# Optimization experiments

Measured on AMD Instinct MI355X. Metric: run time of the kernel, lower is better.

The kernel has to match this reference:

```python
import jax, jax.numpy as jnp
import numpy as np

D_MODEL = 1024
N_HEADS = 16
HEAD_DIM = D_MODEL // N_HEADS


def setup_inputs() -> dict:
    key = jax.random.key(0)
    ks = jax.random.split(key, 9)
    B, S = 2, 2048
    s = 1.0 / np.sqrt(D_MODEL)
    return {
        "x": jax.random.normal(ks[0], (B, S, D_MODEL), dtype=jnp.float32),
        "Wq": jax.random.normal(ks[1], (D_MODEL, D_MODEL), dtype=jnp.float32) * s,
        "bq": jnp.zeros((D_MODEL,), dtype=jnp.float32),
        "Wk": jax.random.normal(ks[2], (D_MODEL, D_MODEL), dtype=jnp.float32) * s,
        "bk": jnp.zeros((D_MODEL,), dtype=jnp.float32),
        "Wv": jax.random.normal(ks[3], (D_MODEL, D_MODEL), dtype=jnp.float32) * s,
        "bv": jnp.zeros((D_MODEL,), dtype=jnp.float32),
        "Wo": jax.random.normal(ks[4], (D_MODEL, D_MODEL), dtype=jnp.float32) * s,
        "bo": jnp.zeros((D_MODEL,), dtype=jnp.float32),
    }


def _rope_emb(seq_len, dtype):
    # inv_freq over even dims of head_dim; emb = cat(freqs, freqs)
    inv_freq = 1.0 / (10000.0 ** (jnp.arange(0, HEAD_DIM, 2, dtype=jnp.float32) / HEAD_DIM))
    t = jnp.arange(seq_len, dtype=jnp.float32)
    freqs = t[:, None] * inv_freq[None, :]          # [S, head_dim/2]
    emb = jnp.concatenate([freqs, freqs], axis=-1)  # [S, head_dim]
    return emb.astype(dtype)[None, None, :, :]       # [1,1,S,head_dim]


def _rotate_half(x):
    x1, x2 = jnp.split(x, 2, axis=-1)
    return jnp.concatenate([-x2, x1], axis=-1)


def _apply_rope(x, emb):
    return x * jnp.cos(emb) + _rotate_half(x) * jnp.sin(emb)


def reference(x, Wq, bq, Wk, bk, Wv, bv, Wo, bo):
    B, S, _ = x.shape
    # projections (torch Linear: x @ W.T + b; here W is stored already as [in,out])
    q = (x @ Wq + bq).reshape(B, S, N_HEADS, HEAD_DIM).transpose(0, 2, 1, 3)
    k = (x @ Wk + bk).reshape(B, S, N_HEADS, HEAD_DIM).transpose(0, 2, 1, 3)
    v = (x @ Wv + bv).reshape(B, S, N_HEADS, HEAD_DIM).transpose(0, 2, 1, 3)
    emb = _rope_emb(S, x.dtype)
    q = _apply_rope(q, emb)
    k = _apply_rope(k, emb)
    scores = jnp.einsum('bhqd,bhkd->bhqk', q, k) / jnp.sqrt(jnp.asarray(HEAD_DIM, x.dtype))
    attn = jax.nn.softmax(scores, axis=-1)
    out = jnp.einsum('bhqk,bhkd->bhqd', attn, v)
    out = out.transpose(0, 2, 1, 3).reshape(B, S, D_MODEL)
    return out @ Wo + bo
```

## Files before the change

kernel.cpp:

```cpp
#include <hip/hip_runtime.h>
#include <hip/hip_bf16.h>
#include <math.h>

#define SEQ 2048
#define DM 1024
#define NH 16
#define HD 64
#define NBH 32
#define MTOT 4096

typedef __attribute__((ext_vector_type(8))) short short8;
typedef __attribute__((ext_vector_type(4))) float floatx4;
typedef __attribute__((ext_vector_type(8))) unsigned short u16x8;
typedef __attribute__((ext_vector_type(4))) unsigned short u16x4;

__device__ __forceinline__ unsigned short f2bf(float f) {
    unsigned int u = __float_as_uint(f);
    u += 0x7FFFu + ((u >> 16) & 1u);
    return (unsigned short)(u >> 16);
}

#define AS1C const __attribute__((address_space(1))) void*
#define AS3  __attribute__((address_space(3))) void*

#define QSCALE 0.18033688011112042f

__global__ __launch_bounds__(256) void cvt_x_kernel(
    const float* __restrict__ x, unsigned short* __restrict__ xb)
{
    size_t base = ((size_t)blockIdx.x * 256 + threadIdx.x) * 8;
    float4 a = *(const float4*)(x + base);
    float4 b = *(const float4*)(x + base + 4);
    u16x8 o;
    o[0]=f2bf(a.x); o[1]=f2bf(a.y); o[2]=f2bf(a.z); o[3]=f2bf(a.w);
    o[4]=f2bf(b.x); o[5]=f2bf(b.y); o[6]=f2bf(b.z); o[7]=f2bf(b.w);
    *(u16x8*)(xb + base) = o;
}

__global__ __launch_bounds__(256) void cvt_w_kernel(
    const float* __restrict__ Wq, const float* __restrict__ Wk,
    const float* __restrict__ Wv, const float* __restrict__ Wo,
    unsigned short* __restrict__ Wt)
{
    __shared__ float Ls[64][65];
    const int z = blockIdx.z;
    const float* src = (z==0) ? Wq : (z==1) ? Wk : (z==2) ? Wv : Wo;
    unsigned short* dst = Wt + (size_t)z * DM * DM;
    const int tid = threadIdx.x;
    const int k0 = blockIdx.x * 64, n0 = blockIdx.y * 64;

    int r = tid >> 2, cseg = (tid & 3) * 16;
    #pragma unroll
    for (int e = 0; e < 4; ++e) {
        float4 v = *(const float4*)(src + (size_t)(k0 + r) * DM + n0 + cseg + e*4);
        Ls[r][cseg+e*4+0] = v.x; Ls[r][cseg+e*4+1] = v.y;
        Ls[r][cseg+e*4+2] = v.z; Ls[r][cseg+e*4+3] = v.w;
    }
    __syncthreads();
    int n = tid >> 2, kseg = (tid & 3) * 16;
    #pragma unroll
    for (int half = 0; half < 2; ++half) {
        u16x8 o;
        #pragma unroll
        for (int e = 0; e < 8; ++e) o[e] = f2bf(Ls[kseg + half*8 + e][n]);
        *(u16x8*)(dst + (size_t)(n0 + n) * DM + k0 + kseg + half*8) = o;
    }
}

#define GEMM_CORE(A_, Bt_, m0_, n0_)                                          \
    const int tid = threadIdx.x;                                              \
    const int wave = tid >> 6, lane = tid & 63;                               \
    const int quad = lane >> 4, l16 = lane & 15;                              \
    const int mh = (wave & 1) * 64, nh = (wave >> 1) * 64;                    \
    floatx4 acc[4][4];                                                        \
    _Pragma("unroll")                                                         \
    for (int i = 0; i < 4; ++i)                                               \
        _Pragma("unroll")                                                     \
        for (int j = 0; j < 4; ++j) acc[i][j] = (floatx4){0.f,0.f,0.f,0.f};   \
    {                                                                         \
        const int srow = wave*32 + (lane>>2);                                 \
        const int scol = (lane & 3) * 8;                                      \
        const unsigned short* ga = A_ + (size_t)(m0_ + srow)*DM + scol;       \
        const unsigned short* gb = Bt_ + (size_t)(n0_ + srow)*DM + scol;      \
        char* lA = (char*)As; char* lB = (char*)Bs;                           \
        for (int k0 = 0; k0 < DM; k0 += 32) {                                 \
            __syncthreads();                                                  \
            _Pragma("unroll")                                                 \
            for (int u = 0; u < 2; ++u) {                                     \
                __builtin_amdgcn_global_load_lds(                             \
                    (AS1C)(ga + (size_t)u*16*DM + k0),                        \
                    (AS3)(lA + (wave*32 + u*16)*64), 16, 0, 0);               \
                __builtin_amdgcn_global_load_lds(                             \
                    (AS1C)(gb + (size_t)u*16*DM + k0),                        \
                    (AS3)(lB + (wave*32 + u*16)*64), 16, 0, 0);               \
            }                                                                 \
            __syncthreads();                                                  \
            short8 af[4], bf[4];                                              \
            _Pragma("unroll")                                                 \
            for (int t = 0; t < 4; ++t) {                                     \
                af[t] = *(const short8*)&As[(mh + t*16 + l16)*32 + quad*8];   \
                bf[t] = *(const short8*)&Bs[(nh + t*16 + l16)*32 + quad*8];   \
            }                                                                 \
            _Pragma("unroll")                                                 \
            for (int mt = 0; mt < 4; ++mt)                                    \
                _Pragma("unroll")                                             \
                for (int nt = 0; nt < 4; ++nt)                                \
                    acc[mt][nt] = __builtin_amdgcn_mfma_f32_16x16x32_bf16(    \
                        af[mt], bf[nt], acc[mt][nt], 0, 0, 0);                \
        }                                                                     \
    }

__global__ __launch_bounds__(256, 3) void qkv_gemm_kernel(
    const unsigned short* __restrict__ xb, const unsigned short* __restrict__ Wt,
    const float* __restrict__ bq, const float* __restrict__ bk,
    const float* __restrict__ bv,
    unsigned short* __restrict__ qb, unsigned short* __restrict__ kb,
    unsigned short* __restrict__ vtg)
{
    __shared__ unsigned short As[128*32];
    __shared__ unsigned short Bs[128*32];
    const int z = blockIdx.z;
    const unsigned short* Bt = Wt + (size_t)z * DM * DM;
    const float* bias = (z==0) ? bq : (z==1) ? bk : bv;
    const int m0 = blockIdx.x * 128, n0 = blockIdx.y * 128;

    GEMM_CORE(xb, Bt, m0, n0)

    float bb[4];
    #pragma unroll
    for (int nt = 0; nt < 4; ++nt) bb[nt] = bias[n0 + nh + nt*16 + l16];

    if (z == 2) {
        unsigned short* Tw = (wave & 1) ? Bs : As;
        const int b = m0 >> 11;
        const int bufsel = tid >> 7, nl = tid & 127;
        const int ng = n0 + nl, hh = ng >> 6, dhh = ng & 63;
        unsigned short* vrow = vtg + ((size_t)((b*NH + hh)*HD + dhh))*SEQ;
        #pragma unroll
        for (int t = 0; t < 4; ++t) {
            __syncthreads();
            #pragma unroll
            for (int nt = 0; nt < 4; ++nt)
                #pragma unroll
                for (int r = 0; r < 4; ++r)
                    Tw[(nh + nt*16 + l16)*24 + quad*4 + r] =
                        f2bf(acc[t][nt][r] + bb[nt]);
            __syncthreads();
            const unsigned short* T2 = bufsel ? Bs : As;
            int sbase = (m0 & 2047) + bufsel*64 + t*16;
            int t32 = (sbase >> 4) & 1;
            int sb32 = sbase & ~31;
            #pragma unroll
            for (int gq = 0; gq < 4; ++gq) {
                u16x4 v4 = *(const u16x4*)&T2[nl*24 + gq*4];
                *(u16x4*)(vrow + sb32 + gq*8 + t32*4) = v4;
            }
        }
    } else {
        unsigned short* outh = (z==0) ? qb : kb;
        const float scl = (z == 0) ? QSCALE : 1.0f;
        const int h = (n0 + nh) >> 6;
        float inv0 = __expf(-(float)l16        * 0.28782313662425572f);
        float inv1 = __expf(-(float)(l16 + 16) * 0.28782313662425572f);
        #pragma unroll
        for (int mt = 0; mt < 4; ++mt)
            #pragma unroll
            for (int r = 0; r < 4; ++r) {
                int m = m0 + mh + mt*16 + quad*4 + r;
                int b = m >> 11, s = m & (SEQ-1);
                float s0, c0, s1, c1;
                __sincosf((float)s * inv0, &s0, &c0);
                __sincosf((float)s * inv1, &s1, &c1);
                float a0 = acc[mt][0][r] + bb[0];
                float a1 = acc[mt][1][r] + bb[1];
                float a2 = acc[mt][2][r] + bb[2];
                float a3 = acc[mt][3][r] + bb[3];
                u16x4 o;
                o[0] = f2bf((a0*c0 - a2*s0) * scl);
                o[1] = f2bf((a1*c1 - a3*s1) * scl);
                o[2] = f2bf((a2*c0 + a0*s0) * scl);
                o[3] = f2bf((a3*c1 + a1*s1) * scl);
                *(u16x4*)(outh + ((size_t)((b*NH + h)*SEQ + s))*HD + 4*l16) = o;
            }
    }
}

__global__ __launch_bounds__(256, 3) void out_gemm_kernel(
    const unsigned short* __restrict__ ctxb, const unsigned short* __restrict__ Wto,
    const float* __restrict__ bo, float* __restrict__ outf)
{
    __shared__ unsigned short As[128*32];
    __shared__ unsigned short Bs[128*32];
    const int m0 = blockIdx.x * 128, n0 = blockIdx.y * 128;

    GEMM_CORE(ctxb, Wto, m0, n0)

    float bb[4];
    #pragma unroll
    for (int nt = 0; nt < 4; ++nt) bb[nt] = bo[n0 + nh + nt*16 + l16];
    #pragma unroll
    for (int mt = 0; mt < 4; ++mt)
        #pragma unroll
        for (int r = 0; r < 4; ++r) {
            int m = m0 + mh + mt*16 + quad*4 + r;
            #pragma unroll
            for (int nt = 0; nt < 4; ++nt) {
                int n = n0 + nh + nt*16 + l16;
                outf[(size_t)m*DM + n] = acc[mt][nt][r] + bb[nt];
            }
        }
}

__global__ __launch_bounds__(256, 2) void attn_mfma_kernel(
    const unsigned short* __restrict__ Q, const unsigned short* __restrict__ K,
    const unsigned short* __restrict__ Vtg, unsigned short* __restrict__ ctxb)
{
    __shared__ unsigned short Ks[2*128*32];
    __shared__ unsigned short Vt[4*64*32];
    __shared__ float Lred[4][32];

    const int tid  = threadIdx.x;
    const int wave = tid >> 6, lane = tid & 63;
    const int quad = lane >> 4, l16 = lane & 15;
    const int bh = blockIdx.x & 31;
    const int qt = blockIdx.x >> 5;

    const unsigned short* Qb = Q + (size_t)bh * SEQ * HD;
    const unsigned short* Kb = K + (size_t)bh * SEQ * HD;
    const unsigned short* Vb = Vtg + (size_t)bh * HD * SEQ;

    short8 qf[2][2];
    #pragma unroll
    for (int qg = 0; qg < 2; ++qg) {
        const unsigned short* qrow =
            Qb + (size_t)(qt*128 + wave*32 + qg*16 + l16)*HD;
        qf[qg][0] = *(const short8*)(qrow + quad*8);
        qf[qg][1] = *(const short8*)(qrow + 32 + quad*8);
    }

    const unsigned short* gsrc[8];
    char* ldst[8];
    int step;
    if (wave < 2) {
        #pragma unroll
        for (int u = 0; u < 8; ++u) {
            int G = u*128 + wave*64 + lane;
            int gl = G & 3, key = (G >> 2) & 127, s = G >> 9;
            gsrc[u] = Kb + (size_t)key*HD + s*32 + (gl ^ ((key>>2)&3))*8;
            ldst[u] = (char*)Ks + G*16;
        }
        step = 128*HD;
    } else {
        #pragma unroll
        for (int u = 0; u < 8; ++u) {
            int G = u*128 + (wave-2)*64 + lane;
            int gl = G & 3, d = (G >> 2) & 63, g = G >> 8;
            gsrc[u] = Vb + (size_t)d*SEQ + g*32 + (gl ^ ((d>>2)&3))*8;
            ldst[u] = (char*)Vt + G*16;
        }
        step = 128;
    }

    float l_p[2] = {0.f, 0.f};
    floatx4 Oacc[2][4];
    #pragma unroll
    for (int qg = 0; qg < 2; ++qg)
        #pragma unroll
        for (int dt = 0; dt < 4; ++dt) Oacc[qg][dt] = (floatx4){0.f,0.f,0.f,0.f};

    const int swz = (quad ^ (l16 >> 2)) * 8;

    for (int kt = 0; kt < SEQ/128; ++kt) {
        __syncthreads();
        #pragma unroll
        for (int u = 0; u < 8; ++u)
            __builtin_amdgcn_global_load_lds((AS1C)gsrc[u], (AS3)ldst[u], 16, 0, 0);
        #pragma unroll
        for (int u = 0; u < 8; ++u) gsrc[u] += step;
        __syncthreads();

        #pragma unroll
        for (int g = 0; g < 4; ++g) {
            floatx4 Sc[2][2];
            #pragma unroll
            for (int t = 0; t < 2; ++t)
                #pragma unroll
                for (int qg = 0; qg < 2; ++qg) Sc[t][qg] = (floatx4){0.f,0.f,0.f,0.f};
            #pragma unroll
            for (int t = 0; t < 2; ++t) {
                const int c = g*2 + t;
                #pragma unroll
                for (int s = 0; s < 2; ++s) {
                    short8 af = *(const short8*)&Ks[s*4096 + (c*16 + l16)*32 + swz];
                    #pragma unroll
                    for (int qg = 0; qg < 2; ++qg)
                        Sc[t][qg] = __builtin_amdgcn_mfma_f32_16x16x32_bf16(
                            af, qf[qg][s], Sc[t][qg], 0, 0, 0);
                }
            }
            short8 a8[2];
            #pragma unroll
            for (int qg = 0; qg < 2; ++qg) {
                float p[8];
                #pragma unroll
                for (int t = 0; t < 2; ++t)
                    #pragma unroll
                    for (int r = 0; r < 4; ++r) p[t*4+r] = exp2f(Sc[t][qg][r]);
                l_p[qg] += ((p[0]+p[1]) + (p[2]+p[3])) + ((p[4]+p[5]) + (p[6]+p[7]));
                u16x8 av;
                #pragma unroll
                for (int e = 0; e < 4; ++e) {
                    __hip_bfloat162 w = __float22bfloat162_rn(make_float2(p[2*e], p[2*e+1]));
                    unsigned int uu; __builtin_memcpy(&uu, &w, 4);
                    av[2*e]   = (unsigned short)(uu & 0xFFFF);
                    av[2*e+1] = (unsigned short)(uu >> 16);
                }
                __builtin_memcpy(&a8[qg], &av, 16);
            }
            #pragma unroll
            for (int dt = 0; dt < 4; ++dt) {
                short8 bf = *(const short8*)&Vt[g*2048 + (dt*16 + l16)*32 + swz];
                #pragma unroll
                for (int qg = 0; qg < 2; ++qg)
                    Oacc[qg][dt] = __builtin_amdgcn_mfma_f32_16x16x32_bf16(
                        a8[qg], bf, Oacc[qg][dt], 0, 0, 0);
            }
        }
    }

    #pragma unroll
    for (int qg = 0; qg < 2; ++qg) {
        l_p[qg] += __shfl_xor(l_p[qg], 16);
        l_p[qg] += __shfl_xor(l_p[qg], 32);
        Lred[wave][qg*16 + l16] = l_p[qg];
    }

    int b = bh >> 4, h = bh & 15;
    #pragma unroll
    for (int qg = 0; qg < 2; ++qg)
        #pragma unroll
        for (int r = 0; r < 4; ++r) {
            int sr = qt*128 + wave*32 + qg*16 + quad*4 + r;
            float invl = 1.0f / Lred[wave][qg*16 + quad*4 + r];
            unsigned short* dst = ctxb + ((size_t)(b*SEQ + sr))*DM + h*HD;
            #pragma unroll
            for (int dt = 0; dt < 4; ++dt)
                dst[dt*16 + l16] = f2bf(Oacc[qg][dt][r] * invl);
        }
}

extern "C" void kernel_launch(void* const* d_in, const int* in_sizes, int n_in,
                              void* d_out, int out_size, void* d_ws, size_t ws_size,
                              hipStream_t stream) {
    const float* x  = (const float*)d_in[0];
    const float* Wq = (const float*)d_in[1];
    const float* bq = (const float*)d_in[2];
    const float* Wk = (const float*)d_in[3];
    const float* bk = (const float*)d_in[4];
    const float* Wv = (const float*)d_in[5];
    const float* bv = (const float*)d_in[6];
    const float* Wo = (const float*)d_in[7];
    const float* bo = (const float*)d_in[8];
    float* out = (float*)d_out;

    char* ws = (char*)d_ws;
    unsigned short* xb   = (unsigned short*)(ws);
    unsigned short* Wt   = (unsigned short*)(ws +  8u*1024*1024);
    unsigned short* qb   = (unsigned short*)(ws + 16u*1024*1024);
    unsigned short* kb   = (unsigned short*)(ws + 24u*1024*1024);
    unsigned short* vtg  = (unsigned short*)(ws + 32u*1024*1024);
    unsigned short* ctxb = (unsigned short*)(ws + 40u*1024*1024);

    cvt_x_kernel<<<(MTOT*DM/8)/256, 256, 0, stream>>>(x, xb);
    cvt_w_kernel<<<dim3(DM/64, DM/64, 4), 256, 0, stream>>>(Wq, Wk, Wv, Wo, Wt);

    qkv_gemm_kernel<<<dim3(MTOT/128, DM/128, 3), 256, 0, stream>>>(
        xb, Wt, bq, bk, bv, qb, kb, vtg);

    attn_mfma_kernel<<<512, 256, 0, stream>>>(qb, kb, vtg, ctxb);

    out_gemm_kernel<<<dim3(MTOT/128, DM/128), 256, 0, stream>>>(
        ctxb, Wt + (size_t)3*DM*DM, bo, out);
    (void)in_sizes; (void)n_in; (void)out_size; (void)ws_size;
}
```

Baseline: 206.1 us.

## Double-buffer K/V tiles in attention and widen GEMM k-step to 64

The attention kernel now holds two 32KB K/V LDS buffers. It prefetches the next 128-key tile via global_load_lds while computing on the current one, which drops one barrier per iteration. The projection GEMMs load two 32-wide k-chunks per barrier pair, halving the number of synchronizations. Both changes raise LDS use per block, which can lower occupancy. The compiler may also insert conservative vmcnt waits that remove the intended load/compute overlap.

```diff
diff --git a/kernel.cpp b/kernel.cpp
--- a/kernel.cpp
+++ b/kernel.cpp
@@ -83,30 +83,35 @@
         const unsigned short* ga = A_ + (size_t)(m0_ + srow)*DM + scol;       \
         const unsigned short* gb = Bt_ + (size_t)(n0_ + srow)*DM + scol;      \
         char* lA = (char*)As; char* lB = (char*)Bs;                           \
-        for (int k0 = 0; k0 < DM; k0 += 32) {                                 \
+        for (int k0 = 0; k0 < DM; k0 += 64) {                                 \
             __syncthreads();                                                  \
             _Pragma("unroll")                                                 \
-            for (int u = 0; u < 2; ++u) {                                     \
-                __builtin_amdgcn_global_load_lds(                             \
-                    (AS1C)(ga + (size_t)u*16*DM + k0),                        \
-                    (AS3)(lA + (wave*32 + u*16)*64), 16, 0, 0);               \
-                __builtin_amdgcn_global_load_lds(                             \
-                    (AS1C)(gb + (size_t)u*16*DM + k0),                        \
-                    (AS3)(lB + (wave*32 + u*16)*64), 16, 0, 0);               \
+            for (int ch = 0; ch < 2; ++ch)                                    \
+                _Pragma("unroll")                                             \
+                for (int u = 0; u < 2; ++u) {                                 \
+                    __builtin_amdgcn_global_load_lds(                         \
+                        (AS1C)(ga + (size_t)u*16*DM + k0 + ch*32),            \
+                        (AS3)(lA + ch*8192 + (wave*32 + u*16)*64), 16, 0, 0); \
+                    __builtin_amdgcn_global_load_lds(                         \
+                        (AS1C)(gb + (size_t)u*16*DM + k0 + ch*32),            \
+                        (AS3)(lB + ch*8192 + (wave*32 + u*16)*64), 16, 0, 0); \
+                }                                                             \
+            __syncthreads();                                                  \
+            _Pragma("unroll")                                                 \
+            for (int ch = 0; ch < 2; ++ch) {                                  \
+                short8 af[4], bf[4];                                          \
+                _Pragma("unroll")                                             \
+                for (int t = 0; t < 4; ++t) {                                 \
+                    af[t] = *(const short8*)&As[ch][(mh + t*16 + l16)*32 + quad*8]; \
+                    bf[t] = *(const short8*)&Bs[ch][(nh + t*16 + l16)*32 + quad*8]; \
+                }                                                             \
+                _Pragma("unroll")                                             \
+                for (int mt = 0; mt < 4; ++mt)                                \
+                    _Pragma("unroll")                                         \
+                    for (int nt = 0; nt < 4; ++nt)                            \
+                        acc[mt][nt] = __builtin_amdgcn_mfma_f32_16x16x32_bf16(\
+                            af[mt], bf[nt], acc[mt][nt], 0, 0, 0);            \
             }                                                                 \
-            __syncthreads();                                                  \
-            short8 af[4], bf[4];                                              \
-            _Pragma("unroll")                                                 \
-            for (int t = 0; t < 4; ++t) {                                     \
-                af[t] = *(const short8*)&As[(mh + t*16 + l16)*32 + quad*8];   \
-                bf[t] = *(const short8*)&Bs[(nh + t*16 + l16)*32 + quad*8];   \
-            }                                                                 \
-            _Pragma("unroll")                                                 \
-            for (int mt = 0; mt < 4; ++mt)                                    \
-                _Pragma("unroll")                                             \
-                for (int nt = 0; nt < 4; ++nt)                                \
-                    acc[mt][nt] = __builtin_amdgcn_mfma_f32_16x16x32_bf16(    \
-                        af[mt], bf[nt], acc[mt][nt], 0, 0, 0);                \
         }                                                                     \
     }
 
@@ -117,8 +122,8 @@
     unsigned short* __restrict__ qb, unsigned short* __restrict__ kb,
     unsigned short* __restrict__ vtg)
 {
-    __shared__ unsigned short As[128*32];
-    __shared__ unsigned short Bs[128*32];
+    __shared__ unsigned short As[2][128*32];
+    __shared__ unsigned short Bs[2][128*32];
     const int z = blockIdx.z;
     const unsigned short* Bt = Wt + (size_t)z * DM * DM;
     const float* bias = (z==0) ? bq : (z==1) ? bk : bv;
@@ -131,7 +136,7 @@
     for (int nt = 0; nt < 4; ++nt) bb[nt] = bias[n0 + nh + nt*16 + l16];
 
     if (z == 2) {
-        unsigned short* Tw = (wave & 1) ? Bs : As;
+        unsigned short* Tw = (wave & 1) ? (unsigned short*)Bs : (unsigned short*)As;
         const int b = m0 >> 11;
         const int bufsel = tid >> 7, nl = tid & 127;
         const int ng = n0 + nl, hh = ng >> 6, dhh = ng & 63;
@@ -146,7 +151,8 @@
                     Tw[(nh + nt*16 + l16)*24 + quad*4 + r] =
                         f2bf(acc[t][nt][r] + bb[nt]);
             __syncthreads();
-            const unsigned short* T2 = bufsel ? Bs : As;
+            const unsigned short* T2 = bufsel ? (const unsigned short*)Bs
+                                              : (const unsigned short*)As;
             int sbase = (m0 & 2047) + bufsel*64 + t*16;
             int t32 = (sbase >> 4) & 1;
             int sb32 = sbase & ~31;
@@ -189,8 +195,8 @@
     const unsigned short* __restrict__ ctxb, const unsigned short* __restrict__ Wto,
     const float* __restrict__ bo, float* __restrict__ outf)
 {
-    __shared__ unsigned short As[128*32];
-    __shared__ unsigned short Bs[128*32];
+    __shared__ unsigned short As[2][128*32];
+    __shared__ unsigned short Bs[2][128*32];
     const int m0 = blockIdx.x * 128, n0 = blockIdx.y * 128;
 
     GEMM_CORE(ctxb, Wto, m0, n0)
@@ -215,8 +221,7 @@
     const unsigned short* __restrict__ Q, const unsigned short* __restrict__ K,
     const unsigned short* __restrict__ Vtg, unsigned short* __restrict__ ctxb)
 {
-    __shared__ unsigned short Ks[2*128*32];
-    __shared__ unsigned short Vt[4*64*32];
+    __shared__ unsigned short KVs[2][16384];
     __shared__ float Lred[4][32];
 
     const int tid  = threadIdx.x;
@@ -239,7 +244,7 @@
     }
 
     const unsigned short* gsrc[8];
-    char* ldst[8];
+    int loff[8];
     int step;
     if (wave < 2) {
         #pragma unroll
@@ -247,7 +252,7 @@
             int G = u*128 + wave*64 + lane;
             int gl = G & 3, key = (G >> 2) & 127, s = G >> 9;
             gsrc[u] = Kb + (size_t)key*HD + s*32 + (gl ^ ((key>>2)&3))*8;
-            ldst[u] = (char*)Ks + G*16;
+            loff[u] = G*16;
         }
         step = 128*HD;
     } else {
@@ -256,10 +261,11 @@
             int G = u*128 + (wave-2)*64 + lane;
             int gl = G & 3, d = (G >> 2) & 63, g = G >> 8;
             gsrc[u] = Vb + (size_t)d*SEQ + g*32 + (gl ^ ((d>>2)&3))*8;
-            ldst[u] = (char*)Vt + G*16;
+            loff[u] = 16384 + G*16;
         }
         step = 128;
     }
+    char* lbase = (char*)KVs;
 
     float l_p[2] = {0.f, 0.f};
     floatx4 Oacc[2][4];
@@ -270,14 +276,24 @@
 
     const int swz = (quad ^ (l16 >> 2)) * 8;
 
+    #pragma unroll
+    for (int u = 0; u < 8; ++u)
+        __builtin_amdgcn_global_load_lds((AS1C)gsrc[u], (AS3)(lbase + loff[u]), 16, 0, 0);
+    #pragma unroll
+    for (int u = 0; u < 8; ++u) gsrc[u] += step;
+
     for (int kt = 0; kt < SEQ/128; ++kt) {
         __syncthreads();
-        #pragma unroll
-        for (int u = 0; u < 8; ++u)
-            __builtin_amdgcn_global_load_lds((AS1C)gsrc[u], (AS3)ldst[u], 16, 0, 0);
-        #pragma unroll
-        for (int u = 0; u < 8; ++u) gsrc[u] += step;
-        __syncthreads();
+        if (kt + 1 < SEQ/128) {
+            char* nb = lbase + ((kt + 1) & 1) * 32768;
+            #pragma unroll
+            for (int u = 0; u < 8; ++u)
+                __builtin_amdgcn_global_load_lds((AS1C)gsrc[u], (AS3)(nb + loff[u]), 16, 0, 0);
+            #pragma unroll
+            for (int u = 0; u < 8; ++u) gsrc[u] += step;
+        }
+        const unsigned short* Kbuf = KVs[kt & 1];
+        const unsigned short* Vbuf = KVs[kt & 1] + 8192;
 
         #pragma unroll
         for (int g = 0; g < 4; ++g) {
@@ -291,7 +307,7 @@
                 const int c = g*2 + t;
                 #pragma unroll
                 for (int s = 0; s < 2; ++s) {
-                    short8 af = *(const short8*)&Ks[s*4096 + (c*16 + l16)*32 + swz];
+                    short8 af = *(const short8*)&Kbuf[s*4096 + (c*16 + l16)*32 + swz];
                     #pragma unroll
                     for (int qg = 0; qg < 2; ++qg)
                         Sc[t][qg] = __builtin_amdgcn_mfma_f32_16x16x32_bf16(
@@ -319,7 +335,7 @@
             }
             #pragma unroll
             for (int dt = 0; dt < 4; ++dt) {
-                short8 bf = *(const short8*)&Vt[g*2048 + (dt*16 + l16)*32 + swz];
+                short8 bf = *(const short8*)&Vbuf[g*2048 + (dt*16 + l16)*32 + swz];
                 #pragma unroll
                 for (int qg = 0; qg < 2; ++qg)
                     Oacc[qg][dt] = __builtin_amdgcn_mfma_f32_16x16x32_bf16(
```

Measured after the change: 210.2 us. About the same (+2.0%).

## Split attention over key halves with smaller blocks and a combine kernel

Applied to the files above, without the earlier changes.

The attention kernel now uses 128-thread blocks handling 64 queries each and splits the key sequence into two halves, launching 2048 blocks instead of 512. Each block writes unnormalised partial outputs in bf16 plus row sums, and a new combine kernel adds the two halves and normalises into ctx. The aim is more parallelism and occupancy for the attention stage. The cost is an extra kernel launch, extra global traffic for the partials, and bf16 rounding of the partial sums. The row-sum buffer reuses the x workspace, which is only safe because xb is no longer needed by then.

```diff
diff --git a/kernel.cpp b/kernel.cpp
--- a/kernel.cpp
+++ b/kernel.cpp
@@ -18,6 +18,10 @@
     unsigned int u = __float_as_uint(f);
     u += 0x7FFFu + ((u >> 16) & 1u);
     return (unsigned short)(u >> 16);
+}
+__device__ __forceinline__ float bf2f(unsigned short h) {
+    unsigned int u = (unsigned int)h << 16;
+    return __uint_as_float(u);
 }
 
 #define AS1C const __attribute__((address_space(1))) void*
@@ -211,54 +215,45 @@
         }
 }
 
-__global__ __launch_bounds__(256, 2) void attn_mfma_kernel(
+__global__ __launch_bounds__(128, 4) void attn_mfma_kernel(
     const unsigned short* __restrict__ Q, const unsigned short* __restrict__ K,
-    const unsigned short* __restrict__ Vtg, unsigned short* __restrict__ ctxb)
-{
-    __shared__ unsigned short Ks[2*128*32];
-    __shared__ unsigned short Vt[4*64*32];
-    __shared__ float Lred[4][32];
+    const unsigned short* __restrict__ Vtg,
+    unsigned short* __restrict__ Opart, float* __restrict__ Lpart)
+{
+    __shared__ unsigned short KVs[16384];
 
     const int tid  = threadIdx.x;
     const int wave = tid >> 6, lane = tid & 63;
     const int quad = lane >> 4, l16 = lane & 15;
-    const int bh = blockIdx.x & 31;
-    const int qt = blockIdx.x >> 5;
+    const int bh   = blockIdx.x & 31;
+    const int qt   = (blockIdx.x >> 5) & 31;
+    const int half = blockIdx.x >> 10;
 
     const unsigned short* Qb = Q + (size_t)bh * SEQ * HD;
-    const unsigned short* Kb = K + (size_t)bh * SEQ * HD;
-    const unsigned short* Vb = Vtg + (size_t)bh * HD * SEQ;
+    const unsigned short* Kb = K + (size_t)bh * SEQ * HD + (size_t)half*1024*HD;
+    const unsigned short* Vb = Vtg + (size_t)bh * HD * SEQ + half*1024;
 
     short8 qf[2][2];
     #pragma unroll
     for (int qg = 0; qg < 2; ++qg) {
         const unsigned short* qrow =
-            Qb + (size_t)(qt*128 + wave*32 + qg*16 + l16)*HD;
+            Qb + (size_t)(qt*64 + wave*32 + qg*16 + l16)*HD;
         qf[qg][0] = *(const short8*)(qrow + quad*8);
         qf[qg][1] = *(const short8*)(qrow + 32 + quad*8);
     }
 
-    const unsigned short* gsrc[8];
-    char* ldst[8];
-    int step;
-    if (wave < 2) {
-        #pragma unroll
-        for (int u = 0; u < 8; ++u) {
-            int G = u*128 + wave*64 + lane;
-            int gl = G & 3, key = (G >> 2) & 127, s = G >> 9;
-            gsrc[u] = Kb + (size_t)key*HD + s*32 + (gl ^ ((key>>2)&3))*8;
-            ldst[u] = (char*)Ks + G*16;
-        }
-        step = 128*HD;
+    const int gX = ((lane & 3) ^ ((lane >> 4) & 3)) * 8;
+    const unsigned short* gbase;
+    int ldsbase;
+    int gstep;
+    if (wave == 0) {
+        gbase = Kb + (size_t)(lane >> 2)*HD + gX;
+        ldsbase = lane*16;
+        gstep = 128*HD;
     } else {
-        #pragma unroll
-        for (int u = 0; u < 8; ++u) {
-            int G = u*128 + (wave-2)*64 + lane;
-            int gl = G & 3, d = (G >> 2) & 63, g = G >> 8;
-            gsrc[u] = Vb + (size_t)d*SEQ + g*32 + (gl ^ ((d>>2)&3))*8;
-            ldst[u] = (char*)Vt + G*16;
-        }
-        step = 128;
+        gbase = Vb + (size_t)(lane >> 2)*SEQ + gX;
+        ldsbase = 16384 + lane*16;
+        gstep = 128;
     }
 
     float l_p[2] = {0.f, 0.f};
@@ -270,14 +265,26 @@
 
     const int swz = (quad ^ (l16 >> 2)) * 8;
 
-    for (int kt = 0; kt < SEQ/128; ++kt) {
+    for (int kt = 0; kt < 8; ++kt) {
         __syncthreads();
-        #pragma unroll
-        for (int u = 0; u < 8; ++u)
-            __builtin_amdgcn_global_load_lds((AS1C)gsrc[u], (AS3)ldst[u], 16, 0, 0);
-        #pragma unroll
-        for (int u = 0; u < 8; ++u) gsrc[u] += step;
+        if (wave == 0) {
+            #pragma unroll
+            for (int u = 0; u < 16; ++u)
+                __builtin_amdgcn_global_load_lds(
+                    (AS1C)(gbase + (u & 7)*(16*HD) + (u >> 3)*32),
+                    (AS3)((char*)KVs + ldsbase + u*1024), 16, 0, 0);
+        } else {
+            #pragma unroll
+            for (int u = 0; u < 16; ++u)
+                __builtin_amdgcn_global_load_lds(
+                    (AS1C)(gbase + (u & 3)*(16*SEQ) + (u >> 2)*32),
+                    (AS3)((char*)KVs + ldsbase + u*1024), 16, 0, 0);
+        }
+        gbase += gstep;
         __syncthreads();
+
+        const unsigned short* Kbuf = KVs;
+        const unsigned short* Vbuf = KVs + 8192;
 
         #pragma unroll
         for (int g = 0; g < 4; ++g) {
@@ -291,7 +298,7 @@
                 const int c = g*2 + t;
                 #pragma unroll
                 for (int s = 0; s < 2; ++s) {
-                    short8 af = *(const short8*)&Ks[s*4096 + (c*16 + l16)*32 + swz];
+                    short8 af = *(const short8*)&Kbuf[s*4096 + (c*16 + l16)*32 + swz];
                     #pragma unroll
                     for (int qg = 0; qg < 2; ++qg)
                         Sc[t][qg] = __builtin_amdgcn_mfma_f32_16x16x32_bf16(
@@ -319,7 +326,7 @@
             }
             #pragma unroll
             for (int dt = 0; dt < 4; ++dt) {
-                short8 bf = *(const short8*)&Vt[g*2048 + (dt*16 + l16)*32 + swz];
+                short8 bf = *(const short8*)&Vbuf[g*2048 + (dt*16 + l16)*32 + swz];
                 #pragma unroll
                 for (int qg = 0; qg < 2; ++qg)
                     Oacc[qg][dt] = __builtin_amdgcn_mfma_f32_16x16x32_bf16(
@@ -332,21 +339,45 @@
     for (int qg = 0; qg < 2; ++qg) {
         l_p[qg] += __shfl_xor(l_p[qg], 16);
         l_p[qg] += __shfl_xor(l_p[qg], 32);
-        Lred[wave][qg*16 + l16] = l_p[qg];
-    }
-
+    }
+
+    size_t obase = (((size_t)((half*32 + bh)*32 + qt))*64)*64;
+    #pragma unroll
+    for (int qg = 0; qg < 2; ++qg) {
+        #pragma unroll
+        for (int r = 0; r < 4; ++r) {
+            int ql = wave*32 + qg*16 + quad*4 + r;
+            unsigned short* dst = Opart + obase + (size_t)ql*64;
+            #pragma unroll
+            for (int dt = 0; dt < 4; ++dt)
+                dst[dt*16 + l16] = f2bf(Oacc[qg][dt][r]);
+        }
+        if (quad == 0)
+            Lpart[((size_t)(half*32 + bh))*SEQ + qt*64 + wave*32 + qg*16 + l16] = l_p[qg];
+    }
+}
+
+__global__ __launch_bounds__(256) void attn_combine_kernel(
+    const unsigned short* __restrict__ Opart, const float* __restrict__ Lpart,
+    unsigned short* __restrict__ ctxb)
+{
+    const size_t HS = (size_t)32*32*64*64;
+    int idx = blockIdx.x*256 + threadIdx.x;
+    int oct = idx & 7;
+    int q   = (idx >> 3) & (SEQ-1);
+    int bh  = idx >> 14;
+    int qt = q >> 6, ql = q & 63;
+    size_t pbase = ((((size_t)(bh*32 + qt))*64 + ql)*64) + oct*8;
+    u16x8 o1 = *(const u16x8*)(Opart + pbase);
+    u16x8 o2 = *(const u16x8*)(Opart + HS + pbase);
+    float l = Lpart[(size_t)bh*SEQ + q] + Lpart[(size_t)32*SEQ + bh*SEQ + q];
+    float inv = 1.0f / l;
+    u16x8 o;
+    #pragma unroll
+    for (int e = 0; e < 8; ++e)
+        o[e] = f2bf((bf2f(o1[e]) + bf2f(o2[e])) * inv);
     int b = bh >> 4, h = bh & 15;
-    #pragma unroll
-    for (int qg = 0; qg < 2; ++qg)
-        #pragma unroll
-        for (int r = 0; r < 4; ++r) {
-            int sr = qt*128 + wave*32 + qg*16 + quad*4 + r;
-            float invl = 1.0f / Lred[wave][qg*16 + quad*4 + r];
-            unsigned short* dst = ctxb + ((size_t)(b*SEQ + sr))*DM + h*HD;
-            #pragma unroll
-            for (int dt = 0; dt < 4; ++dt)
-                dst[dt*16 + l16] = f2bf(Oacc[qg][dt][r] * invl);
-        }
+    *(u16x8*)(ctxb + ((size_t)(b*SEQ + q))*DM + h*HD + oct*8) = o;
 }
 
 extern "C" void kernel_launch(void* const* d_in, const int* in_sizes, int n_in,
@@ -370,6 +401,8 @@
     unsigned short* kb   = (unsigned short*)(ws + 24u*1024*1024);
     unsigned short* vtg  = (unsigned short*)(ws + 32u*1024*1024);
     unsigned short* ctxb = (unsigned short*)(ws + 40u*1024*1024);
+    unsigned short* Op   = (unsigned short*)(ws + 48u*1024*1024);
+    float*          Lp   = (float*)(ws);
 
     cvt_x_kernel<<<(MTOT*DM/8)/256, 256, 0, stream>>>(x, xb);
     cvt_w_kernel<<<dim3(DM/64, DM/64, 4), 256, 0, stream>>>(Wq, Wk, Wv, Wo, Wt);
@@ -377,7 +410,8 @@
     qkv_gemm_kernel<<<dim3(MTOT/128, DM/128, 3), 256, 0, stream>>>(
         xb, Wt, bq, bk, bv, qb, kb, vtg);
 
-    attn_mfma_kernel<<<512, 256, 0, stream>>>(qb, kb, vtg, ctxb);
+    attn_mfma_kernel<<<2048, 128, 0, stream>>>(qb, kb, vtg, Op, Lp);
+    attn_combine_kernel<<<2048, 256, 0, stream>>>(Op, Lp, ctxb);
 
     out_gemm_kernel<<<dim3(MTOT/128, DM/128), 256, 0, stream>>>(
         ctxb, Wt + (size_t)3*DM*DM, bo, out);
```

Result: slower. 232.5 us (+12.8%).

## Split attention over key halves with a combine kernel; fuse conversion kernels

Applied to the files above, without the earlier changes.

The attention kernel now splits the key sequence into two halves and launches twice as many blocks. Each block writes unnormalized bf16 partial outputs and row sums to workspace, and a new combine kernel adds the halves, normalizes, and writes the context. This is meant to give more blocks to balance across compute units. In exchange it adds an extra kernel launch, extra global traffic for the partials, and an extra bf16 rounding step. Separately, the x and weight conversion kernels are merged into one launch to cut launch overhead.

```diff
diff --git a/kernel.cpp b/kernel.cpp
--- a/kernel.cpp
+++ b/kernel.cpp
@@ -19,35 +19,39 @@
     u += 0x7FFFu + ((u >> 16) & 1u);
     return (unsigned short)(u >> 16);
 }
+__device__ __forceinline__ float bf2f(unsigned short h) {
+    unsigned int u = (unsigned int)h << 16;
+    return __uint_as_float(u);
+}
 
 #define AS1C const __attribute__((address_space(1))) void*
 #define AS3  __attribute__((address_space(3))) void*
 
 #define QSCALE 0.18033688011112042f
 
-__global__ __launch_bounds__(256) void cvt_x_kernel(
-    const float* __restrict__ x, unsigned short* __restrict__ xb)
-{
-    size_t base = ((size_t)blockIdx.x * 256 + threadIdx.x) * 8;
-    float4 a = *(const float4*)(x + base);
-    float4 b = *(const float4*)(x + base + 4);
-    u16x8 o;
-    o[0]=f2bf(a.x); o[1]=f2bf(a.y); o[2]=f2bf(a.z); o[3]=f2bf(a.w);
-    o[4]=f2bf(b.x); o[5]=f2bf(b.y); o[6]=f2bf(b.z); o[7]=f2bf(b.w);
-    *(u16x8*)(xb + base) = o;
-}
-
-__global__ __launch_bounds__(256) void cvt_w_kernel(
+__global__ __launch_bounds__(256) void cvt_xw_kernel(
+    const float* __restrict__ x, unsigned short* __restrict__ xb,
     const float* __restrict__ Wq, const float* __restrict__ Wk,
     const float* __restrict__ Wv, const float* __restrict__ Wo,
     unsigned short* __restrict__ Wt)
 {
+    if (blockIdx.x < 2048) {
+        size_t base = ((size_t)blockIdx.x * 256 + threadIdx.x) * 8;
+        float4 a = *(const float4*)(x + base);
+        float4 b = *(const float4*)(x + base + 4);
+        u16x8 o;
+        o[0]=f2bf(a.x); o[1]=f2bf(a.y); o[2]=f2bf(a.z); o[3]=f2bf(a.w);
+        o[4]=f2bf(b.x); o[5]=f2bf(b.y); o[6]=f2bf(b.z); o[7]=f2bf(b.w);
+        *(u16x8*)(xb + base) = o;
+        return;
+    }
     __shared__ float Ls[64][65];
-    const int z = blockIdx.z;
+    const int bid = blockIdx.x - 2048;
+    const int z = bid >> 8;
     const float* src = (z==0) ? Wq : (z==1) ? Wk : (z==2) ? Wv : Wo;
     unsigned short* dst = Wt + (size_t)z * DM * DM;
     const int tid = threadIdx.x;
-    const int k0 = blockIdx.x * 64, n0 = blockIdx.y * 64;
+    const int k0 = (bid & 15) * 64, n0 = ((bid >> 4) & 15) * 64;
 
     int r = tid >> 2, cseg = (tid & 3) * 16;
     #pragma unroll
@@ -213,21 +217,22 @@
 
 __global__ __launch_bounds__(256, 2) void attn_mfma_kernel(
     const unsigned short* __restrict__ Q, const unsigned short* __restrict__ K,
-    const unsigned short* __restrict__ Vtg, unsigned short* __restrict__ ctxb)
+    const unsigned short* __restrict__ Vtg,
+    unsigned short* __restrict__ Opart, float* __restrict__ Lpart)
 {
     __shared__ unsigned short Ks[2*128*32];
     __shared__ unsigned short Vt[4*64*32];
-    __shared__ float Lred[4][32];
 
     const int tid  = threadIdx.x;
     const int wave = tid >> 6, lane = tid & 63;
     const int quad = lane >> 4, l16 = lane & 15;
-    const int bh = blockIdx.x & 31;
-    const int qt = blockIdx.x >> 5;
+    const int bh   = blockIdx.x & 31;
+    const int qt   = (blockIdx.x >> 5) & 15;
+    const int half = blockIdx.x >> 9;
 
     const unsigned short* Qb = Q + (size_t)bh * SEQ * HD;
-    const unsigned short* Kb = K + (size_t)bh * SEQ * HD;
-    const unsigned short* Vb = Vtg + (size_t)bh * HD * SEQ;
+    const unsigned short* Kb = K + (size_t)bh * SEQ * HD + (size_t)half*1024*HD;
+    const unsigned short* Vb = Vtg + (size_t)bh * HD * SEQ + half*1024;
 
     short8 qf[2][2];
     #pragma unroll
@@ -270,7 +275,7 @@
 
     const int swz = (quad ^ (l16 >> 2)) * 8;
 
-    for (int kt = 0; kt < SEQ/128; ++kt) {
+    for (int kt = 0; kt < 8; ++kt) {
         __syncthreads();
         #pragma unroll
         for (int u = 0; u < 8; ++u)
@@ -332,21 +337,46 @@
     for (int qg = 0; qg < 2; ++qg) {
         l_p[qg] += __shfl_xor(l_p[qg], 16);
         l_p[qg] += __shfl_xor(l_p[qg], 32);
-        Lred[wave][qg*16 + l16] = l_p[qg];
-    }
-
+    }
+
+    size_t obase = (((size_t)((half*32 + bh)*16 + qt))*128)*64;
+    #pragma unroll
+    for (int qg = 0; qg < 2; ++qg) {
+        #pragma unroll
+        for (int r = 0; r < 4; ++r) {
+            int ql = wave*32 + qg*16 + quad*4 + r;
+            unsigned short* dst = Opart + obase + (size_t)ql*64;
+            #pragma unroll
+            for (int dt = 0; dt < 4; ++dt)
+                dst[dt*16 + l16] = f2bf(Oacc[qg][dt][r]);
+        }
+        if (quad == 0)
+            Lpart[((size_t)(half*32 + bh))*SEQ + qt*128 + wave*32 + qg*16 + l16]
+                = l_p[qg];
+    }
+}
+
+__global__ __launch_bounds__(256) void attn_combine_kernel(
+    const unsigned short* __restrict__ Opart, const float* __restrict__ Lpart,
+    unsigned short* __restrict__ ctxb)
+{
+    const size_t HS = (size_t)32*16*128*64;
+    int idx = blockIdx.x*256 + threadIdx.x;
+    int oct = idx & 7;
+    int q   = (idx >> 3) & (SEQ-1);
+    int bh  = idx >> 14;
+    int qt = q >> 7, ql = q & 127;
+    size_t pbase = ((((size_t)(bh*16 + qt))*128 + ql)*64) + oct*8;
+    u16x8 o1 = *(const u16x8*)(Opart + pbase);
+    u16x8 o2 = *(const u16x8*)(Opart + HS + pbase);
+    float l = Lpart[(size_t)bh*SEQ + q] + Lpart[(size_t)32*SEQ + bh*SEQ + q];
+    float inv = 1.0f / l;
+    u16x8 o;
+    #pragma unroll
+    for (int e = 0; e < 8; ++e)
+        o[e] = f2bf((bf2f(o1[e]) + bf2f(o2[e])) * inv);
     int b = bh >> 4, h = bh & 15;
-    #pragma unroll
-    for (int qg = 0; qg < 2; ++qg)
-        #pragma unroll
-        for (int r = 0; r < 4; ++r) {
-            int sr = qt*128 + wave*32 + qg*16 + quad*4 + r;
-            float invl = 1.0f / Lred[wave][qg*16 + quad*4 + r];
-            unsigned short* dst = ctxb + ((size_t)(b*SEQ + sr))*DM + h*HD;
-            #pragma unroll
-            for (int dt = 0; dt < 4; ++dt)
-                dst[dt*16 + l16] = f2bf(Oacc[qg][dt][r] * invl);
-        }
+    *(u16x8*)(ctxb + ((size_t)(b*SEQ + q))*DM + h*HD + oct*8) = o;
 }
 
 extern "C" void kernel_launch(void* const* d_in, const int* in_sizes, int n_in,
@@ -370,14 +400,16 @@
     unsigned short* kb   = (unsigned short*)(ws + 24u*1024*1024);
     unsigned short* vtg  = (unsigned short*)(ws + 32u*1024*1024);
     unsigned short* ctxb = (unsigned short*)(ws + 40u*1024*1024);
-
-    cvt_x_kernel<<<(MTOT*DM/8)/256, 256, 0, stream>>>(x, xb);
-    cvt_w_kernel<<<dim3(DM/64, DM/64, 4), 256, 0, stream>>>(Wq, Wk, Wv, Wo, Wt);
+    unsigned short* Op   = (unsigned short*)(ws + 48u*1024*1024);
+    float*          Lp   = (float*)(ws);
+
+    cvt_xw_kernel<<<3072, 256, 0, stream>>>(x, xb, Wq, Wk, Wv, Wo, Wt);
 
     qkv_gemm_kernel<<<dim3(MTOT/128, DM/128, 3), 256, 0, stream>>>(
         xb, Wt, bq, bk, bv, qb, kb, vtg);
 
-    attn_mfma_kernel<<<512, 256, 0, stream>>>(qb, kb, vtg, ctxb);
+    attn_mfma_kernel<<<1024, 256, 0, stream>>>(qb, kb, vtg, Op, Lp);
+    attn_combine_kernel<<<2048, 256, 0, stream>>>(Op, Lp, ctxb);
 
     out_gemm_kernel<<<dim3(MTOT/128, DM/128), 256, 0, stream>>>(
         ctxb, Wt + (size_t)3*DM*DM, bo, out);
```

Measured after the change: 203.7 us. No clear change (-1.2%).
